# Performance work log

Measured on AMD Instinct MI355X. Metric: run time of the kernel, lower is better.

## Reference

```python
import jax, jax.numpy as jnp
import numpy as np

N = 100000   # nodes
E = 1600000  # edges
D = 128      # input = hidden channels
L = 4        # 1 + num_convs GIN layers
G = 512      # graphs in batch
BN_EPS = 1e-5


def setup_inputs() -> dict:
    key = jax.random.key(0)
    ks = jax.random.split(key, 10)
    s = 1.0 / np.sqrt(D)
    x = jax.random.normal(ks[0], (N, D), jnp.float32)
    edge_index = jax.random.randint(ks[1], (2, E), 0, N)
    batch = jnp.sort(jax.random.randint(ks[2], (N,), 0, G))
    return {
        "x": x,
        "edge_index": edge_index,
        "batch": batch,
        "W1": jax.random.normal(ks[3], (L, D, D), jnp.float32) * s,
        "b1": jnp.zeros((L, D), jnp.float32),
        "gamma": jnp.ones((L, D), jnp.float32),
        "beta": jnp.zeros((L, D), jnp.float32),
        "W2": jax.random.normal(ks[4], (L, D, D), jnp.float32) * s,
        "b2": jnp.zeros((L, D), jnp.float32),
        "lin_W": jax.random.normal(ks[5], (D, 2), jnp.float32) * s,
        "lin_b": jnp.zeros((2,), jnp.float32),
    }


def reference(x, edge_index, batch, W1, b1, gamma, beta, W2, b2, lin_W, lin_b):
    src, dst = edge_index[0], edge_index[1]
    h = x
    for l in range(L):
        # GINConv, eps=0: (1+eps)*x_i + sum_{j->i} x_j  (scatter-add over edges)
        agg = jax.ops.segment_sum(h[src], dst, num_segments=N)  # [N, D]
        z = h + agg
        # MLP: Linear -> BatchNorm1d (training stats) -> ELU -> Linear -> ELU
        z = z @ W1[l] + b1[l]
        mu = jnp.mean(z, axis=0)
        var = jnp.mean((z - mu) ** 2, axis=0)  # biased var, as torch BN
        z = (z - mu) * jax.lax.rsqrt(var + BN_EPS) * gamma[l] + beta[l]
        z = jax.nn.elu(z)
        h = jax.nn.elu(z @ W2[l] + b2[l])
    # global_mean_pool: per-graph segment mean
    sums = jax.ops.segment_sum(h, batch, num_segments=G)             # [G, D]
    cnt = jax.ops.segment_sum(jnp.ones((N, 1), h.dtype), batch, num_segments=G)
    pooled = sums / jnp.maximum(cnt, 1.0)
    return pooled @ lin_W + lin_b  # [G, 2]
```

## Files before the change

### kernel.cpp

```cpp
#include <hip/hip_runtime.h>
#include <cstdint>

#define D 128
#define BKT_SHIFT 8
#define BKT_CAP 5120
#define EDGES_PER_BLOCK 4096
#define NREP 8

typedef __attribute__((ext_vector_type(4))) float floatx4;
typedef __attribute__((ext_vector_type(4))) _Float16 half4;
typedef __attribute__((ext_vector_type(8))) _Float16 half8;

__device__ __forceinline__ float elu_f(float x) {
    return x > 0.0f ? x : __expf(x) - 1.0f;
}

__global__ void init_cursor_kernel(int* __restrict__ gcursor, int NB) {
    int t = blockIdx.x * 256 + threadIdx.x;
    if (t < NB) gcursor[t] = t * BKT_CAP;
}

__global__ __launch_bounds__(256) void bucket_scatter_kernel(
    const int* __restrict__ src, const int* __restrict__ dst,
    int* __restrict__ gcursor, int2* __restrict__ staging, int E, int NB) {
    __shared__ int lcnt[512];
    __shared__ int lbase[512];
    int t = threadIdx.x;
    lcnt[t] = 0; lcnt[t + 256] = 0;
    __syncthreads();
    int base = blockIdx.x * EDGES_PER_BLOCK;
    int s_[16], d_[16], r_[16];
#pragma unroll
    for (int i = 0; i < 16; ++i) {
        int idx = base + i * 256 + t;
        if (idx < E) {
            s_[i] = src[idx];
            d_[i] = dst[idx];
            r_[i] = atomicAdd(&lcnt[d_[i] >> BKT_SHIFT], 1);
        }
    }
    __syncthreads();
    for (int b = t; b < NB; b += 256) {
        int c = lcnt[b];
        if (c) lbase[b] = atomicAdd(&gcursor[b], c);
    }
    __syncthreads();
#pragma unroll
    for (int i = 0; i < 16; ++i) {
        int idx = base + i * 256 + t;
        if (idx < E) {
            int bkt = d_[i] >> BKT_SHIFT;
            staging[lbase[bkt] + r_[i]] = make_int2(s_[i], d_[i]);
        }
    }
}

__global__ __launch_bounds__(256) void bucket_build_kernel(
    const int2* __restrict__ staging, const int* __restrict__ gcursor,
    int* __restrict__ rowstart, int* __restrict__ rowend,
    int* __restrict__ col, int N) {
    __shared__ int hcnt[256];
    __shared__ int hoff[256];
    int t = threadIdx.x;
    int node0 = blockIdx.x << BKT_SHIFT;
    int off0 = blockIdx.x * BKT_CAP;
    int off1 = gcursor[blockIdx.x];
    hcnt[t] = 0;
    __syncthreads();
    for (int i = off0 + t; i < off1; i += 256)
        atomicAdd(&hcnt[staging[i].y - node0], 1);
    __syncthreads();
    int deg = hcnt[t];
    hoff[t] = deg;
    __syncthreads();
    for (int off = 1; off < 256; off <<= 1) {
        int u = (t >= off) ? hoff[t - off] : 0;
        __syncthreads();
        hoff[t] += u;
        __syncthreads();
    }
    int myoff = (t == 0) ? 0 : hoff[t - 1];
    __syncthreads();
    hoff[t] = myoff;
    hcnt[t] = 0;
    if (node0 + t < N) {
        rowstart[node0 + t] = off0 + myoff;
        rowend[node0 + t] = off0 + myoff + deg;
    }
    __syncthreads();
    for (int i = off0 + t; i < off1; i += 256) {
        int2 p = staging[i];
        int dl = p.y - node0;
        int pos = off0 + hoff[dl] + atomicAdd(&hcnt[dl], 1);
        col[pos] = p.x;
    }
}

__global__ void to_half_kernel(const float* __restrict__ in, _Float16* __restrict__ outp, int n4) {
    int i = blockIdx.x * 256 + threadIdx.x;
    if (i >= n4) return;
    float4 v = ((const float4*)in)[i];
    half4 h = {(_Float16)v.x, (_Float16)v.y, (_Float16)v.z, (_Float16)v.w};
    ((half4*)outp)[i] = h;
}

__global__ void wprep_kernel(const float* __restrict__ W1, const float* __restrict__ W2,
                             _Float16* __restrict__ Wph, _Float16* __restrict__ Wpl,
                             int total) {
    int idx = blockIdx.x * 256 + threadIdx.x;
    if (idx >= total) return;
    int mat = idx >> 14;
    int rem = idx & 16383;
    int tile = rem >> 9;
    int lane = (rem >> 3) & 63;
    int j = rem & 7;
    int ks = tile >> 3, nt = tile & 7;
    int n = nt * 16 + (lane & 15);
    int k = ks * 32 + (lane >> 4) * 8 + j;
    int l = mat >> 1;
    const float* W = (mat & 1) ? W2 : W1;
    float v = W[(size_t)l * D * D + k * D + n];
    _Float16 h = (_Float16)v;
    _Float16 lo = (_Float16)(v - (float)h);
    Wph[idx] = h;
    Wpl[idx] = lo;
}

template <bool GATHER, bool ELU_OUT, bool STATS, int MW>
__global__ __launch_bounds__(256, MW) void gemm_mfma(
    const _Float16* __restrict__ Hh,
    const int* __restrict__ rowstart, const int* __restrict__ rowend,
    const int* __restrict__ col,
    const _Float16* __restrict__ Z,
    const _Float16* __restrict__ Wph, const _Float16* __restrict__ Wpl,
    const float* __restrict__ bias,
    const float* __restrict__ colsum_in, const float* __restrict__ gamma,
    const float* __restrict__ beta,
    _Float16* __restrict__ outp16, float* __restrict__ colsum_out, int N) {
    __shared__ _Float16 sA[64 * 136];
    __shared__ float bnsum[2 * D];
    __shared__ float s_sc[D];
    __shared__ float s_sh[D];
    const int tid = threadIdx.x;
    const int row0 = blockIdx.x * 64;

    if (STATS && tid < 2 * D) bnsum[tid] = 0.f;

    if (GATHER) {
        const int rg = tid >> 4;
        const int q = tid & 15;
        const half8* hh8 = (const half8*)Hh;
#pragma unroll
        for (int i = 0; i < 4; ++i) {
            int r = rg * 4 + i;
            int node = row0 + r;
            float a0 = 0.f, a1 = 0.f, a2 = 0.f, a3 = 0.f;
            float a4 = 0.f, a5 = 0.f, a6 = 0.f, a7 = 0.f;
            if (node < N) {
                half8 sf = hh8[(uint32_t)(node * 16 + q)];
                a0 = (float)sf[0]; a1 = (float)sf[1]; a2 = (float)sf[2]; a3 = (float)sf[3];
                a4 = (float)sf[4]; a5 = (float)sf[5]; a6 = (float)sf[6]; a7 = (float)sf[7];
                int e0 = rowstart[node], e1 = rowend[node];
                int e = e0;
                for (; e + 15 < e1; e += 16) {
                    int j0 = col[e],      j1 = col[e + 1],  j2 = col[e + 2],  j3 = col[e + 3];
                    int j4 = col[e + 4],  j5 = col[e + 5],  j6 = col[e + 6],  j7 = col[e + 7];
                    int j8 = col[e + 8],  j9 = col[e + 9],  jA = col[e + 10], jB = col[e + 11];
                    int jC = col[e + 12], jD = col[e + 13], jE = col[e + 14], jF = col[e + 15];
                    half8 v0 = hh8[(uint32_t)(j0 * 16 + q)];
                    half8 v1 = hh8[(uint32_t)(j1 * 16 + q)];
                    half8 v2 = hh8[(uint32_t)(j2 * 16 + q)];
                    half8 v3 = hh8[(uint32_t)(j3 * 16 + q)];
                    half8 v4 = hh8[(uint32_t)(j4 * 16 + q)];
                    half8 v5 = hh8[(uint32_t)(j5 * 16 + q)];
                    half8 v6 = hh8[(uint32_t)(j6 * 16 + q)];
                    half8 v7 = hh8[(uint32_t)(j7 * 16 + q)];
                    half8 v8 = hh8[(uint32_t)(j8 * 16 + q)];
                    half8 v9 = hh8[(uint32_t)(j9 * 16 + q)];
                    half8 vA = hh8[(uint32_t)(jA * 16 + q)];
                    half8 vB = hh8[(uint32_t)(jB * 16 + q)];
                    half8 vC = hh8[(uint32_t)(jC * 16 + q)];
                    half8 vD = hh8[(uint32_t)(jD * 16 + q)];
                    half8 vE = hh8[(uint32_t)(jE * 16 + q)];
                    half8 vF = hh8[(uint32_t)(jF * 16 + q)];
#pragma unroll
                    for (int c = 0; c < 8; ++c) {
                        float s = (((float)v0[c] + (float)v1[c]) + ((float)v2[c] + (float)v3[c]))
                                + (((float)v4[c] + (float)v5[c]) + ((float)v6[c] + (float)v7[c]))
                                + (((float)v8[c] + (float)v9[c]) + ((float)vA[c] + (float)vB[c]))
                                + (((float)vC[c] + (float)vD[c]) + ((float)vE[c] + (float)vF[c]));
                        if (c == 0) a0 += s; else if (c == 1) a1 += s;
                        else if (c == 2) a2 += s; else if (c == 3) a3 += s;
                        else if (c == 4) a4 += s; else if (c == 5) a5 += s;
                        else if (c == 6) a6 += s; else a7 += s;
                    }
                }
                if (e + 7 < e1) {
                    int j0 = col[e],     j1 = col[e + 1], j2 = col[e + 2], j3 = col[e + 3];
                    int j4 = col[e + 4], j5 = col[e + 5], j6 = col[e + 6], j7 = col[e + 7];
                    half8 v0 = hh8[(uint32_t)(j0 * 16 + q)];
                    half8 v1 = hh8[(uint32_t)(j1 * 16 + q)];
                    half8 v2 = hh8[(uint32_t)(j2 * 16 + q)];
                    half8 v3 = hh8[(uint32_t)(j3 * 16 + q)];
                    half8 v4 = hh8[(uint32_t)(j4 * 16 + q)];
                    half8 v5 = hh8[(uint32_t)(j5 * 16 + q)];
                    half8 v6 = hh8[(uint32_t)(j6 * 16 + q)];
                    half8 v7 = hh8[(uint32_t)(j7 * 16 + q)];
                    a0 += (((float)v0[0] + (float)v1[0]) + ((float)v2[0] + (float)v3[0]))
                        + (((float)v4[0] + (float)v5[0]) + ((float)v6[0] + (float)v7[0]));
                    a1 += (((float)v0[1] + (float)v1[1]) + ((float)v2[1] + (float)v3[1]))
                        + (((float)v4[1] + (float)v5[1]) + ((float)v6[1] + (float)v7[1]));
                    a2 += (((float)v0[2] + (float)v1[2]) + ((float)v2[2] + (float)v3[2]))
                        + (((float)v4[2] + (float)v5[2]) + ((float)v6[2] + (float)v7[2]));
                    a3 += (((float)v0[3] + (float)v1[3]) + ((float)v2[3] + (float)v3[3]))
                        + (((float)v4[3] + (float)v5[3]) + ((float)v6[3] + (float)v7[3]));
                    a4 += (((float)v0[4] + (float)v1[4]) + ((float)v2[4] + (float)v3[4]))
                        + (((float)v4[4] + (float)v5[4]) + ((float)v6[4] + (float)v7[4]));
                    a5 += (((float)v0[5] + (float)v1[5]) + ((float)v2[5] + (float)v3[5]))
                        + (((float)v4[5] + (float)v5[5]) + ((float)v6[5] + (float)v7[5]));
                    a6 += (((float)v0[6] + (float)v1[6]) + ((float)v2[6] + (float)v3[6]))
                        + (((float)v4[6] + (float)v5[6]) + ((float)v6[6] + (float)v7[6]));
                    a7 += (((float)v0[7] + (float)v1[7]) + ((float)v2[7] + (float)v3[7]))
                        + (((float)v4[7] + (float)v5[7]) + ((float)v6[7] + (float)v7[7]));
                    e += 8;
                }
                if (e < e1) {
                    int last = e1 - 1;
                    int e0c = e,     e1c = e + 1 > last ? last : e + 1;
                    int e2c = e + 2 > last ? last : e + 2, e3c = e + 3 > last ? last : e + 3;
                    int e4c = e + 4 > last ? last : e + 4, e5c = e + 5 > last ? last : e + 5;
                    int e6c = e + 6 > last ? last : e + 6, e7c = e + 7 > last ? last : e + 7;
                    int j0 = col[e0c], j1 = col[e1c], j2 = col[e2c], j3 = col[e3c];
                    int j4 = col[e4c], j5 = col[e5c], j6 = col[e6c], j7 = col[e7c];
                    float m1 = (e + 1 <= last) ? 1.f : 0.f, m2 = (e + 2 <= last) ? 1.f : 0.f;
                    float m3 = (e + 3 <= last) ? 1.f : 0.f, m4 = (e + 4 <= last) ? 1.f : 0.f;
                    float m5 = (e + 5 <= last) ? 1.f : 0.f, m6 = (e + 6 <= last) ? 1.f : 0.f;
                    float m7 = (e + 7 <= last) ? 1.f : 0.f;
                    half8 v0 = hh8[(uint32_t)(j0 * 16 + q)];
                    half8 v1 = hh8[(uint32_t)(j1 * 16 + q)];
                    half8 v2 = hh8[(uint32_t)(j2 * 16 + q)];
                    half8 v3 = hh8[(uint32_t)(j3 * 16 + q)];
                    half8 v4 = hh8[(uint32_t)(j4 * 16 + q)];
                    half8 v5 = hh8[(uint32_t)(j5 * 16 + q)];
                    half8 v6 = hh8[(uint32_t)(j6 * 16 + q)];
                    half8 v7 = hh8[(uint32_t)(j7 * 16 + q)];
                    a0 += (float)v0[0] + m1 * (float)v1[0] + m2 * (float)v2[0] + m3 * (float)v3[0]
                        + m4 * (float)v4[0] + m5 * (float)v5[0] + m6 * (float)v6[0] + m7 * (float)v7[0];
                    a1 += (float)v0[1] + m1 * (float)v1[1] + m2 * (float)v2[1] + m3 * (float)v3[1]
                        + m4 * (float)v4[1] + m5 * (float)v5[1] + m6 * (float)v6[1] + m7 * (float)v7[1];
                    a2 += (float)v0[2] + m1 * (float)v1[2] + m2 * (float)v2[2] + m3 * (float)v3[2]
                        + m4 * (float)v4[2] + m5 * (float)v5[2] + m6 * (float)v6[2] + m7 * (float)v7[2];
                    a3 += (float)v0[3] + m1 * (float)v1[3] + m2 * (float)v2[3] + m3 * (float)v3[3]
                        + m4 * (float)v4[3] + m5 * (float)v5[3] + m6 * (float)v6[3] + m7 * (float)v7[3];
                    a4 += (float)v0[4] + m1 * (float)v1[4] + m2 * (float)v2[4] + m3 * (float)v3[4]
                        + m4 * (float)v4[4] + m5 * (float)v5[4] + m6 * (float)v6[4] + m7 * (float)v7[4];
                    a5 += (float)v0[5] + m1 * (float)v1[5] + m2 * (float)v2[5] + m3 * (float)v3[5]
                        + m4 * (float)v4[5] + m5 * (float)v5[5] + m6 * (float)v6[5] + m7 * (float)v7[5];
                    a6 += (float)v0[6] + m1 * (float)v1[6] + m2 * (float)v2[6] + m3 * (float)v3[6]
                        + m4 * (float)v4[6] + m5 * (float)v5[6] + m6 * (float)v6[6] + m7 * (float)v7[6];
                    a7 += (float)v0[7] + m1 * (float)v1[7] + m2 * (float)v2[7] + m3 * (float)v3[7]
                        + m4 * (float)v4[7] + m5 * (float)v5[7] + m6 * (float)v6[7] + m7 * (float)v7[7];
                }
            }
            half8 hv = {(_Float16)a0, (_Float16)a1, (_Float16)a2, (_Float16)a3,
                        (_Float16)a4, (_Float16)a5, (_Float16)a6, (_Float16)a7};
            *(half8*)&sA[r * 136 + q * 8] = hv;
        }
    } else {
        if (tid < D) {
            float s = 0.f, s2 = 0.f;
#pragma unroll
            for (int rp = 0; rp < NREP; ++rp) {
                s  += colsum_in[rp * 2 * D + tid];
                s2 += colsum_in[rp * 2 * D + D + tid];
            }
            float invN = 1.0f / (float)N;
            float mu = s * invN;
            float var = s2 * invN - mu * mu;
            float rs = rsqrtf(var + 1e-5f);
            float sc = gamma[tid] * rs;
            s_sc[tid] = sc;
            s_sh[tid] = beta[tid] - mu * sc;
        }
        __syncthreads();
#pragma unroll
        for (int it = 0; it < 4; ++it) {
            int idx = tid + it * 256;
            int r = idx >> 4;
            int q8 = (idx & 15) * 8;
            int gr = row0 + r;
            half8 z = {};
            if (gr < N) z = *(const half8*)&Z[(size_t)gr * D + q8];
            float v0 = elu_f((float)z[0] * s_sc[q8 + 0] + s_sh[q8 + 0]);
            float v1 = elu_f((float)z[1] * s_sc[q8 + 1] + s_sh[q8 + 1]);
            float v2 = elu_f((float)z[2] * s_sc[q8 + 2] + s_sh[q8 + 2]);
            float v3 = elu_f((float)z[3] * s_sc[q8 + 3] + s_sh[q8 + 3]);
            float v4 = elu_f((float)z[4] * s_sc[q8 + 4] + s_sh[q8 + 4]);
            float v5 = elu_f((float)z[5] * s_sc[q8 + 5] + s_sh[q8 + 5]);
            float v6 = elu_f((float)z[6] * s_sc[q8 + 6] + s_sh[q8 + 6]);
            float v7 = elu_f((float)z[7] * s_sc[q8 + 7] + s_sh[q8 + 7]);
            half8 hv = {(_Float16)v0, (_Float16)v1, (_Float16)v2, (_Float16)v3,
                        (_Float16)v4, (_Float16)v5, (_Float16)v6, (_Float16)v7};
            *(half8*)&sA[r * 136 + q8] = hv;
        }
    }
    __syncthreads();

    const int wave = tid >> 6, lane = tid & 63;
    const int wm = wave >> 1, wn = wave & 1;
    const int l15 = lane & 15, quad = lane >> 4;
    const half8* bph = (const half8*)Wph;
    const half8* bpl = (const half8*)Wpl;

    floatx4 acc[2][4];
#pragma unroll
    for (int mt = 0; mt < 2; ++mt)
#pragma unroll
        for (int nt = 0; nt < 4; ++nt)
            acc[mt][nt] = (floatx4){0.f, 0.f, 0.f, 0.f};

#pragma unroll
    for (int ks = 0; ks < 4; ++ks) {
        const int kf = ks * 32 + quad * 8;
        half8 ah[2];
#pragma unroll
        for (int mt = 0; mt < 2; ++mt)
            ah[mt] = *(const half8*)&sA[(wm * 32 + mt * 16 + l15) * 136 + kf];
#pragma unroll
        for (int nt = 0; nt < 4; ++nt) {
            int tIdx = (ks * 8 + wn * 4 + nt) * 64 + lane;
            half8 bh = bph[tIdx];
            half8 bl = bpl[tIdx];
            acc[0][nt] = __builtin_amdgcn_mfma_f32_16x16x32_f16(ah[0], bh, acc[0][nt], 0, 0, 0);
            acc[1][nt] = __builtin_amdgcn_mfma_f32_16x16x32_f16(ah[1], bh, acc[1][nt], 0, 0, 0);
            acc[0][nt] = __builtin_amdgcn_mfma_f32_16x16x32_f16(ah[0], bl, acc[0][nt], 0, 0, 0);
            acc[1][nt] = __builtin_amdgcn_mfma_f32_16x16x32_f16(ah[1], bl, acc[1][nt], 0, 0, 0);
        }
    }

#pragma unroll
    for (int nt = 0; nt < 4; ++nt) {
        int c = wn * 64 + nt * 16 + l15;
        float b = bias[c];
        float s = 0.f, s2 = 0.f;
#pragma unroll
        for (int mt = 0; mt < 2; ++mt) {
#pragma unroll
            for (int r = 0; r < 4; ++r) {
                int gm = row0 + wm * 32 + mt * 16 + quad * 4 + r;
                float v = acc[mt][nt][r] + b;
                if (ELU_OUT) v = elu_f(v);
                if (gm < N) {
                    outp16[(size_t)gm * D + c] = (_Float16)v;
                    if (STATS) { s += v; s2 += v * v; }
                }
            }
        }
        if (STATS) {
            atomicAdd(&bnsum[c], s);
            atomicAdd(&bnsum[D + c], s2);
        }
    }
    if (STATS) {
        __syncthreads();
        float* rep = colsum_out + (size_t)(blockIdx.x & (NREP - 1)) * 2 * D;
        if (tid < D) {
            atomicAdd(&rep[tid], bnsum[tid]);
            atomicAdd(&rep[D + tid], bnsum[D + tid]);
        }
    }
}

__global__ __launch_bounds__(128) void pool_kernel(
    const _Float16* __restrict__ h, const int* __restrict__ batch,
    float* __restrict__ pooled, float* __restrict__ cnt, int N) {
    int c = threadIdx.x;
    int r0 = blockIdx.x * 256;
    if (r0 >= N) return;
    int rend = r0 + 256; if (rend > N) rend = N;
    int cur = batch[r0];
    float acc = 0.f;
    float cacc = 0.f;
    for (int r = r0; r < rend; ++r) {
        int b = batch[r];
        if (b != cur) {
            atomicAdd(&pooled[(size_t)cur * D + c], acc);
            if (c == 0) atomicAdd(&cnt[cur], cacc);
            acc = 0.f; cacc = 0.f; cur = b;
        }
        acc += (float)h[(size_t)r * D + c];
        cacc += 1.f;
    }
    atomicAdd(&pooled[(size_t)cur * D + c], acc);
    if (c == 0) atomicAdd(&cnt[cur], cacc);
}

__global__ void final_linear_kernel(const float* __restrict__ pooled,
                                    const float* __restrict__ cnt,
                                    const float* __restrict__ linW,
                                    const float* __restrict__ linb,
                                    float* __restrict__ out, int G) {
    int t = blockIdx.x * blockDim.x + threadIdx.x;
    if (t >= G * 2) return;
    int g = t >> 1, o = t & 1;
    float inv = 1.0f / fmaxf(cnt[g], 1.0f);
    float s = linb[o];
    for (int c = 0; c < D; ++c)
        s += pooled[(size_t)g * D + c] * inv * linW[c * 2 + o];
    out[t] = s;
}

extern "C" void kernel_launch(void* const* d_in, const int* in_sizes, int n_in,
                              void* d_out, int out_size, void* d_ws, size_t ws_size,
                              hipStream_t stream) {
    const float* x      = (const float*)d_in[0];
    const int*  eidx    = (const int*)d_in[1];
    const int*  batch   = (const int*)d_in[2];
    const float* W1     = (const float*)d_in[3];
    const float* b1     = (const float*)d_in[4];
    const float* gamma  = (const float*)d_in[5];
    const float* beta   = (const float*)d_in[6];
    const float* W2     = (const float*)d_in[7];
    const float* b2     = (const float*)d_in[8];
    const float* linW   = (const float*)d_in[9];
    const float* linb   = (const float*)d_in[10];
    float* out = (float*)d_out;

    const int N = in_sizes[0] / D;
    const int E = in_sizes[1] / 2;
    const int L = in_sizes[3] / (D * D);
    const int G = out_size / 2;
    const int* esrc = eidx;
    const int* edst = eidx + E;
    const int NB = (N + 255) >> 8;

    size_t off = 0;
    auto carve = [&](size_t bytes) -> void* {
        void* p = (char*)d_ws + off;
        off += (bytes + 255) & ~(size_t)255;
        return p;
    };
    const size_t ND = (size_t)N * D;
    const int WTOT = 2 * L * D * D;
    _Float16* z16   = (_Float16*)carve(ND * 2);
    _Float16* hhalf = (_Float16*)carve(ND * 2);
    _Float16* Wph = (_Float16*)carve((size_t)WTOT * 2);
    _Float16* Wpl = (_Float16*)carve((size_t)WTOT * 2);
    int* rowstart = (int*)carve((size_t)N * 4);
    int* rowend   = (int*)carve((size_t)N * 4);
    int* col      = (int*)carve((size_t)NB * BKT_CAP * 4);
    float* colsum4 = (float*)carve((size_t)4 * NREP * 2 * D * 4);
    int* gcursor  = (int*)carve(512 * 4);
    float* pooled = (float*)carve((size_t)G * D * 4);
    float* cnt    = (float*)carve((size_t)G * 4);
    int2* staging = (int2*)z16;
    (void)ws_size; (void)n_in;

    hipMemsetAsync(colsum4, 0, (size_t)4 * NREP * 2 * D * 4, stream);
    hipMemsetAsync(pooled, 0, (size_t)G * D * 4 + (size_t)G * 4, stream);

    const int EB = (E + EDGES_PER_BLOCK - 1) / EDGES_PER_BLOCK;
    init_cursor_kernel<<<(NB + 255) / 256, 256, 0, stream>>>(gcursor, NB);
    bucket_scatter_kernel<<<EB, 256, 0, stream>>>(esrc, edst, gcursor, staging, E, NB);
    bucket_build_kernel<<<NB, 256, 0, stream>>>(staging, gcursor, rowstart, rowend, col, N);
    wprep_kernel<<<(WTOT + 255) / 256, 256, 0, stream>>>(W1, W2, Wph, Wpl, WTOT);
    to_half_kernel<<<(int)((ND / 4 + 255) / 256), 256, 0, stream>>>(x, hhalf, (int)(ND / 4));

    const int gemm_grid = (N + 63) / 64;
    for (int l = 0; l < L; ++l) {
        float* colsum = colsum4 + (size_t)l * NREP * 2 * D;
        gemm_mfma<true, false, true, 4><<<gemm_grid, 256, 0, stream>>>(
            hhalf, rowstart, rowend, col, nullptr,
            Wph + (size_t)(l * 2) * D * D, Wpl + (size_t)(l * 2) * D * D,
            b1 + (size_t)l * D, nullptr, nullptr, nullptr, z16, colsum, N);
        gemm_mfma<false, true, false, 8><<<gemm_grid, 256, 0, stream>>>(
            nullptr, nullptr, nullptr, nullptr, z16,
            Wph + (size_t)(l * 2 + 1) * D * D, Wpl + (size_t)(l * 2 + 1) * D * D,
            b2 + (size_t)l * D, colsum, gamma + (size_t)l * D, beta + (size_t)l * D,
            hhalf, nullptr, N);
    }

    pool_kernel<<<(N + 255) / 256, 128, 0, stream>>>(hhalf, batch, pooled, cnt, N);
    final_linear_kernel<<<(G * 2 + 255) / 256, 256, 0, stream>>>(pooled, cnt, linW, linb, out, G);
}
```

Baseline: 662.5 us.

## Fuse prep kernels, stage CSR indices in LDS, fuse mean-pool into last GEMM

Three setup kernels (cursor init, weight split, fp16 conversion) are merged into one launch, and the two memsets become one. The gather GEMM now copies each block's column indices and row offsets into shared memory before gathering, falling back to global memory past the LDS capacity. The final layer's second GEMM writes its output tile to LDS and does the per-graph pooling atomics directly, which removes the pool kernel and one full write and read of h. The extra shared memory could reduce occupancy of the gather GEMM.

```diff
diff --git a/kernel.cpp b/kernel.cpp
--- a/kernel.cpp
+++ b/kernel.cpp
@@ -6,6 +6,7 @@
 #define BKT_CAP 5120
 #define EDGES_PER_BLOCK 4096
 #define NREP 8
+#define LCAP 1536
 
 typedef __attribute__((ext_vector_type(4))) float floatx4;
 typedef __attribute__((ext_vector_type(4))) _Float16 half4;
@@ -13,11 +14,6 @@
 
 __device__ __forceinline__ float elu_f(float x) {
     return x > 0.0f ? x : __expf(x) - 1.0f;
-}
-
-__global__ void init_cursor_kernel(int* __restrict__ gcursor, int NB) {
-    int t = blockIdx.x * 256 + threadIdx.x;
-    if (t < NB) gcursor[t] = t * BKT_CAP;
 }
 
 __global__ __launch_bounds__(256) void bucket_scatter_kernel(
@@ -96,37 +92,44 @@
     }
 }
 
-__global__ void to_half_kernel(const float* __restrict__ in, _Float16* __restrict__ outp, int n4) {
-    int i = blockIdx.x * 256 + threadIdx.x;
-    if (i >= n4) return;
-    float4 v = ((const float4*)in)[i];
-    half4 h = {(_Float16)v.x, (_Float16)v.y, (_Float16)v.z, (_Float16)v.w};
-    ((half4*)outp)[i] = h;
-}
-
-__global__ void wprep_kernel(const float* __restrict__ W1, const float* __restrict__ W2,
-                             _Float16* __restrict__ Wph, _Float16* __restrict__ Wpl,
-                             int total) {
-    int idx = blockIdx.x * 256 + threadIdx.x;
-    if (idx >= total) return;
-    int mat = idx >> 14;
-    int rem = idx & 16383;
-    int tile = rem >> 9;
-    int lane = (rem >> 3) & 63;
-    int j = rem & 7;
-    int ks = tile >> 3, nt = tile & 7;
-    int n = nt * 16 + (lane & 15);
-    int k = ks * 32 + (lane >> 4) * 8 + j;
-    int l = mat >> 1;
-    const float* W = (mat & 1) ? W2 : W1;
-    float v = W[(size_t)l * D * D + k * D + n];
-    _Float16 h = (_Float16)v;
-    _Float16 lo = (_Float16)(v - (float)h);
-    Wph[idx] = h;
-    Wpl[idx] = lo;
-}
-
-template <bool GATHER, bool ELU_OUT, bool STATS, int MW>
+__global__ __launch_bounds__(256) void prep_kernel(
+    const float* __restrict__ x, _Float16* __restrict__ hhalf, int n4,
+    const float* __restrict__ W1, const float* __restrict__ W2,
+    _Float16* __restrict__ Wph, _Float16* __restrict__ Wpl, int wtot,
+    int* __restrict__ gcursor, int NB, int nbh, int nbw) {
+    int bid = blockIdx.x;
+    int t = threadIdx.x;
+    if (bid < nbh) {
+        int i = bid * 256 + t;
+        if (i >= n4) return;
+        float4 v = ((const float4*)x)[i];
+        half4 h = {(_Float16)v.x, (_Float16)v.y, (_Float16)v.z, (_Float16)v.w};
+        ((half4*)hhalf)[i] = h;
+    } else if (bid < nbh + nbw) {
+        int idx = (bid - nbh) * 256 + t;
+        if (idx >= wtot) return;
+        int mat = idx >> 14;
+        int rem = idx & 16383;
+        int tile = rem >> 9;
+        int lane = (rem >> 3) & 63;
+        int j = rem & 7;
+        int ks = tile >> 3, nt = tile & 7;
+        int n = nt * 16 + (lane & 15);
+        int k = ks * 32 + (lane >> 4) * 8 + j;
+        int l = mat >> 1;
+        const float* W = (mat & 1) ? W2 : W1;
+        float v = W[(size_t)l * D * D + k * D + n];
+        _Float16 h = (_Float16)v;
+        _Float16 lo = (_Float16)(v - (float)h);
+        Wph[idx] = h;
+        Wpl[idx] = lo;
+    } else {
+        int i = (bid - nbh - nbw) * 256 + t;
+        if (i < NB) gcursor[i] = i * BKT_CAP;
+    }
+}
+
+template <bool GATHER, bool ELU_OUT, bool STATS, bool POOL, int MW>
 __global__ __launch_bounds__(256, MW) void gemm_mfma(
     const _Float16* __restrict__ Hh,
     const int* __restrict__ rowstart, const int* __restrict__ rowend,
@@ -136,20 +139,37 @@
     const float* __restrict__ bias,
     const float* __restrict__ colsum_in, const float* __restrict__ gamma,
     const float* __restrict__ beta,
-    _Float16* __restrict__ outp16, float* __restrict__ colsum_out, int N) {
+    _Float16* __restrict__ outp16, float* __restrict__ colsum_out,
+    const int* __restrict__ batchg, float* __restrict__ pooled, float* __restrict__ cnt,
+    int N) {
     __shared__ _Float16 sA[64 * 136];
     __shared__ float bnsum[2 * D];
     __shared__ float s_sc[D];
     __shared__ float s_sh[D];
+    __shared__ int lcol[LCAP];
+    __shared__ int srow[65];
     const int tid = threadIdx.x;
     const int row0 = blockIdx.x * 64;
 
     if (STATS && tid < 2 * D) bnsum[tid] = 0.f;
 
     if (GATHER) {
+        const int lastrow = (row0 + 63 < N) ? row0 + 63 : N - 1;
+        const int eb0 = rowstart[row0];
+        const int eb1 = rowend[lastrow];
+        if (tid < 64) {
+            int rr = row0 + tid;
+            srow[tid] = (rr < N) ? rowstart[rr] : eb1;
+        }
+        if (tid == 64) srow[64] = eb1;
+        for (int k = eb0 + tid; k < eb1 && (k - eb0) < LCAP; k += 256)
+            lcol[k - eb0] = col[k];
+        __syncthreads();
+
         const int rg = tid >> 4;
         const int q = tid & 15;
         const half8* hh8 = (const half8*)Hh;
+#define LIDX(ee) ((((ee) - eb0) < LCAP) ? lcol[(ee) - eb0] : col[(ee)])
 #pragma unroll
         for (int i = 0; i < 4; ++i) {
             int r = rg * 4 + i;
@@ -160,13 +180,13 @@
                 half8 sf = hh8[(uint32_t)(node * 16 + q)];
                 a0 = (float)sf[0]; a1 = (float)sf[1]; a2 = (float)sf[2]; a3 = (float)sf[3];
                 a4 = (float)sf[4]; a5 = (float)sf[5]; a6 = (float)sf[6]; a7 = (float)sf[7];
-                int e0 = rowstart[node], e1 = rowend[node];
+                int e0 = srow[r], e1 = srow[r + 1];
                 int e = e0;
                 for (; e + 15 < e1; e += 16) {
-                    int j0 = col[e],      j1 = col[e + 1],  j2 = col[e + 2],  j3 = col[e + 3];
-                    int j4 = col[e + 4],  j5 = col[e + 5],  j6 = col[e + 6],  j7 = col[e + 7];
-                    int j8 = col[e + 8],  j9 = col[e + 9],  jA = col[e + 10], jB = col[e + 11];
-                    int jC = col[e + 12], jD = col[e + 13], jE = col[e + 14], jF = col[e + 15];
+                    int j0 = LIDX(e),      j1 = LIDX(e + 1),  j2 = LIDX(e + 2),  j3 = LIDX(e + 3);
+                    int j4 = LIDX(e + 4),  j5 = LIDX(e + 5),  j6 = LIDX(e + 6),  j7 = LIDX(e + 7);
+                    int j8 = LIDX(e + 8),  j9 = LIDX(e + 9),  jA = LIDX(e + 10), jB = LIDX(e + 11);
+                    int jC = LIDX(e + 12), jD = LIDX(e + 13), jE = LIDX(e + 14), jF = LIDX(e + 15);
                     half8 v0 = hh8[(uint32_t)(j0 * 16 + q)];
                     half8 v1 = hh8[(uint32_t)(j1 * 16 + q)];
                     half8 v2 = hh8[(uint32_t)(j2 * 16 + q)];
@@ -196,8 +216,8 @@
                     }
                 }
                 if (e + 7 < e1) {
-                    int j0 = col[e],     j1 = col[e + 1], j2 = col[e + 2], j3 = col[e + 3];
-                    int j4 = col[e + 4], j5 = col[e + 5], j6 = col[e + 6], j7 = col[e + 7];
+                    int j0 = LIDX(e),     j1 = LIDX(e + 1), j2 = LIDX(e + 2), j3 = LIDX(e + 3);
+                    int j4 = LIDX(e + 4), j5 = LIDX(e + 5), j6 = LIDX(e + 6), j7 = LIDX(e + 7);
                     half8 v0 = hh8[(uint32_t)(j0 * 16 + q)];
                     half8 v1 = hh8[(uint32_t)(j1 * 16 + q)];
                     half8 v2 = hh8[(uint32_t)(j2 * 16 + q)];
@@ -230,8 +250,8 @@
                     int e2c = e + 2 > last ? last : e + 2, e3c = e + 3 > last ? last : e + 3;
                     int e4c = e + 4 > last ? last : e + 4, e5c = e + 5 > last ? last : e + 5;
                     int e6c = e + 6 > last ? last : e + 6, e7c = e + 7 > last ? last : e + 7;
-                    int j0 = col[e0c], j1 = col[e1c], j2 = col[e2c], j3 = col[e3c];
-                    int j4 = col[e4c], j5 = col[e5c], j6 = col[e6c], j7 = col[e7c];
+                    int j0 = LIDX(e0c), j1 = LIDX(e1c), j2 = LIDX(e2c), j3 = LIDX(e3c);
+                    int j4 = LIDX(e4c), j5 = LIDX(e5c), j6 = LIDX(e6c), j7 = LIDX(e7c);
                     float m1 = (e + 1 <= last) ? 1.f : 0.f, m2 = (e + 2 <= last) ? 1.f : 0.f;
                     float m3 = (e + 3 <= last) ? 1.f : 0.f, m4 = (e + 4 <= last) ? 1.f : 0.f;
                     float m5 = (e + 5 <= last) ? 1.f : 0.f, m6 = (e + 6 <= last) ? 1.f : 0.f;
@@ -266,6 +286,7 @@
                         (_Float16)a4, (_Float16)a5, (_Float16)a6, (_Float16)a7};
             *(half8*)&sA[r * 136 + q * 8] = hv;
         }
+#undef LIDX
     } else {
         if (tid < D) {
             float s = 0.f, s2 = 0.f;
@@ -338,6 +359,15 @@
         }
     }
 
+    int* sbatch = (int*)s_sc;
+    if (POOL) {
+        if (tid < 64) {
+            int rr = row0 + tid;
+            sbatch[tid] = (rr < N) ? batchg[rr] : -1;
+        }
+        __syncthreads();
+    }
+
 #pragma unroll
     for (int nt = 0; nt < 4; ++nt) {
         int c = wn * 64 + nt * 16 + l15;
@@ -347,10 +377,13 @@
         for (int mt = 0; mt < 2; ++mt) {
 #pragma unroll
             for (int r = 0; r < 4; ++r) {
-                int gm = row0 + wm * 32 + mt * 16 + quad * 4 + r;
+                int rl = wm * 32 + mt * 16 + quad * 4 + r;
+                int gm = row0 + rl;
                 float v = acc[mt][nt][r] + b;
                 if (ELU_OUT) v = elu_f(v);
-                if (gm < N) {
+                if (POOL) {
+                    if (gm < N) sA[rl * 136 + c] = (_Float16)v;
+                } else if (gm < N) {
                     outp16[(size_t)gm * D + c] = (_Float16)v;
                     if (STATS) { s += v; s2 += v * v; }
                 }
@@ -369,30 +402,31 @@
             atomicAdd(&rep[D + tid], bnsum[D + tid]);
         }
     }
-}
-
-__global__ __launch_bounds__(128) void pool_kernel(
-    const _Float16* __restrict__ h, const int* __restrict__ batch,
-    float* __restrict__ pooled, float* __restrict__ cnt, int N) {
-    int c = threadIdx.x;
-    int r0 = blockIdx.x * 256;
-    if (r0 >= N) return;
-    int rend = r0 + 256; if (rend > N) rend = N;
-    int cur = batch[r0];
-    float acc = 0.f;
-    float cacc = 0.f;
-    for (int r = r0; r < rend; ++r) {
-        int b = batch[r];
-        if (b != cur) {
-            atomicAdd(&pooled[(size_t)cur * D + c], acc);
-            if (c == 0) atomicAdd(&cnt[cur], cacc);
-            acc = 0.f; cacc = 0.f; cur = b;
-        }
-        acc += (float)h[(size_t)r * D + c];
-        cacc += 1.f;
-    }
-    atomicAdd(&pooled[(size_t)cur * D + c], acc);
-    if (c == 0) atomicAdd(&cnt[cur], cacc);
+    if (POOL) {
+        __syncthreads();
+        int c = tid & 127, half = tid >> 7;
+        int rb = half * 32;
+        int cur = -1; float pacc = 0.f; float cc = 0.f;
+        for (int i = 0; i < 32; ++i) {
+            int r = rb + i;
+            int gm = row0 + r;
+            if (gm >= N) break;
+            int g = sbatch[r];
+            if (g != cur) {
+                if (cur >= 0) {
+                    atomicAdd(&pooled[(size_t)cur * D + c], pacc);
+                    if (c == 0) atomicAdd(&cnt[cur], cc);
+                }
+                cur = g; pacc = 0.f; cc = 0.f;
+            }
+            pacc += (float)sA[r * 136 + c];
+            cc += 1.f;
+        }
+        if (cur >= 0) {
+            atomicAdd(&pooled[(size_t)cur * D + c], pacc);
+            if (c == 0) atomicAdd(&cnt[cur], cc);
+        }
+    }
 }
 
 __global__ void final_linear_kernel(const float* __restrict__ pooled,
@@ -449,37 +483,49 @@
     int* rowstart = (int*)carve((size_t)N * 4);
     int* rowend   = (int*)carve((size_t)N * 4);
     int* col      = (int*)carve((size_t)NB * BKT_CAP * 4);
+    const size_t cs_bytes = ((size_t)4 * NREP * 2 * D * 4 + 255) & ~(size_t)255;
+    const size_t pl_bytes = ((size_t)G * D * 4 + 255) & ~(size_t)255;
     float* colsum4 = (float*)carve((size_t)4 * NREP * 2 * D * 4);
-    int* gcursor  = (int*)carve(512 * 4);
-    float* pooled = (float*)carve((size_t)G * D * 4);
-    float* cnt    = (float*)carve((size_t)G * 4);
+    float* pooled  = (float*)carve((size_t)G * D * 4);
+    float* cnt     = (float*)carve((size_t)G * 4);
+    int* gcursor   = (int*)carve(512 * 4);
     int2* staging = (int2*)z16;
     (void)ws_size; (void)n_in;
 
-    hipMemsetAsync(colsum4, 0, (size_t)4 * NREP * 2 * D * 4, stream);
-    hipMemsetAsync(pooled, 0, (size_t)G * D * 4 + (size_t)G * 4, stream);
+    hipMemsetAsync(colsum4, 0, cs_bytes + pl_bytes + (size_t)G * 4, stream);
 
     const int EB = (E + EDGES_PER_BLOCK - 1) / EDGES_PER_BLOCK;
-    init_cursor_kernel<<<(NB + 255) / 256, 256, 0, stream>>>(gcursor, NB);
+    const int n4 = (int)(ND / 4);
+    const int nbh = (n4 + 255) / 256;
+    const int nbw = (WTOT + 255) / 256;
+    const int nbc = (NB + 255) / 256;
+    prep_kernel<<<nbh + nbw + nbc, 256, 0, stream>>>(
+        x, hhalf, n4, W1, W2, Wph, Wpl, WTOT, gcursor, NB, nbh, nbw);
     bucket_scatter_kernel<<<EB, 256, 0, stream>>>(esrc, edst, gcursor, staging, E, NB);
     bucket_build_kernel<<<NB, 256, 0, stream>>>(staging, gcursor, rowstart, rowend, col, N);
-    wprep_kernel<<<(WTOT + 255) / 256, 256, 0, stream>>>(W1, W2, Wph, Wpl, WTOT);
-    to_half_kernel<<<(int)((ND / 4 + 255) / 256), 256, 0, stream>>>(x, hhalf, (int)(ND / 4));
 
     const int gemm_grid = (N + 63) / 64;
     for (int l = 0; l < L; ++l) {
         float* colsum = colsum4 + (size_t)l * NREP * 2 * D;
-        gemm_mfma<true, false, true, 4><<<gemm_grid, 256, 0, stream>>>(
+        gemm_mfma<true, false, true, false, 4><<<gemm_grid, 256, 0, stream>>>(
             hhalf, rowstart, rowend, col, nullptr,
             Wph + (size_t)(l * 2) * D * D, Wpl + (size_t)(l * 2) * D * D,
-            b1 + (size_t)l * D, nullptr, nullptr, nullptr, z16, colsum, N);
-        gemm_mfma<false, true, false, 8><<<gemm_grid, 256, 0, stream>>>(
-            nullptr, nullptr, nullptr, nullptr, z16,
-            Wph + (size_t)(l * 2 + 1) * D * D, Wpl + (size_t)(l * 2 + 1) * D * D,
-            b2 + (size_t)l * D, colsum, gamma + (size_t)l * D, beta + (size_t)l * D,
-            hhalf, nullptr, N);
-    }
-
-    pool_kernel<<<(N + 255) / 256, 128, 0, stream>>>(hhalf, batch, pooled, cnt, N);
+            b1 + (size_t)l * D, nullptr, nullptr, nullptr, z16, colsum,
+            nullptr, nullptr, nullptr, N);
+        if (l < L - 1) {
+            gemm_mfma<false, true, false, false, 8><<<gemm_grid, 256, 0, stream>>>(
+                nullptr, nullptr, nullptr, nullptr, z16,
+                Wph + (size_t)(l * 2 + 1) * D * D, Wpl + (size_t)(l * 2 + 1) * D * D,
+                b2 + (size_t)l * D, colsum, gamma + (size_t)l * D, beta + (size_t)l * D,
+                hhalf, nullptr, nullptr, nullptr, nullptr, N);
+        } else {
+            gemm_mfma<false, true, false, true, 8><<<gemm_grid, 256, 0, stream>>>(
+                nullptr, nullptr, nullptr, nullptr, z16,
+                Wph + (size_t)(l * 2 + 1) * D * D, Wpl + (size_t)(l * 2 + 1) * D * D,
+                b2 + (size_t)l * D, colsum, gamma + (size_t)l * D, beta + (size_t)l * D,
+                nullptr, nullptr, batch, pooled, cnt, N);
+        }
+    }
+
     final_linear_kernel<<<(G * 2 + 255) / 256, 256, 0, stream>>>(pooled, cnt, linW, linb, out, G);
 }
```

Result: faster. 588.7 us (-11.1%).
